# Optimization experiments

Hardware: AMD Instinct MI355X
Metric: run time of the kernel (lower is better)

## Reference

```python
import jax, jax.numpy as jnp
import numpy as np
from jax import lax

ORDER = 6
SAMPLES = 64
TOPK = 512
STRIDE = 2          # contour features are stride-2 w.r.t. input ('1' level)
NMS_THRESH = 0.2
REF_ITERS = 4
REF_MARGIN = 3.0
HC = WC = 256       # contour-feature grid
HF = WF = 512       # full-res (refinement) grid


def conv2d(x, w, b=None, pad=0):
    # x: [B,C,H,W], w: [O,I,kh,kw]
    y = lax.conv_general_dilated(x, w, (1, 1), [(pad, pad), (pad, pad)],
                                 dimension_numbers=("NCHW", "OIHW", "NCHW"))
    if b is not None:
        y = y + b[None, :, None, None]
    return y


def setup_inputs() -> dict:
    key = jax.random.key(0)
    ks = jax.random.split(key, 16)
    s = 0.05
    d = {
        "contour_features": jax.random.normal(ks[0], (4, 64, HC, WC), jnp.float32),
        "enc_score_features": jax.random.normal(ks[1], (4, 64, HC, WC), jnp.float32),
        "refinement_features": jax.random.normal(ks[2], (4, 32, HF, WF), jnp.float32),
        "enc_refinement_features": jax.random.normal(ks[3], (4, 32, HF, WF), jnp.float32),
        # learned params
        "w_score_reduce": jax.random.normal(ks[4], (64, 128, 1, 1)) * s,
        "w_score": jax.random.normal(ks[5], (2, 64, 7, 7)) * s,
        "b_score": jnp.zeros((2,), jnp.float32),
        "w_loc": jax.random.normal(ks[6], (2, 64, 7, 7)) * s,
        "b_loc": jnp.zeros((2,), jnp.float32),
        "w_fourier": jax.random.normal(ks[7], (ORDER * 4, 64, 7, 7)) * s,
        "b_fourier": jnp.zeros((ORDER * 4,), jnp.float32),
        "w_ref_reduce": jax.random.normal(ks[8], (32, 64, 1, 1)) * s,
        "w_ref": jax.random.normal(ks[9], (2, 32, 7, 7)) * s,
        "b_ref": jnp.zeros((2,), jnp.float32),
    }
    return d


def _pairwise_iou(boxes):
    # boxes: [K,4] as (x1,y1,x2,y2)
    x1, y1, x2, y2 = boxes[:, 0], boxes[:, 1], boxes[:, 2], boxes[:, 3]
    area = jnp.maximum(x2 - x1, 0.) * jnp.maximum(y2 - y1, 0.)
    ix1 = jnp.maximum(x1[:, None], x1[None, :])
    iy1 = jnp.maximum(y1[:, None], y1[None, :])
    ix2 = jnp.minimum(x2[:, None], x2[None, :])
    iy2 = jnp.minimum(y2[:, None], y2[None, :])
    inter = jnp.maximum(ix2 - ix1, 0.) * jnp.maximum(iy2 - iy1, 0.)
    union = area[:, None] + area[None, :] - inter
    return inter / jnp.maximum(union, 1e-8)


def _nms_keep(boxes, valid):
    # boxes sorted by descending score. Sequential greedy NMS.
    iou = _pairwise_iou(boxes)  # [K,K]
    idx = jnp.arange(TOPK)

    def body(i, keep):
        sup = (iou[i] > NMS_THRESH) & keep[i] & (idx > i)
        return keep & ~sup

    keep = lax.fori_loop(0, TOPK, body, valid)
    return keep


def _forward(contour_features, enc_score_features, refinement_features,
             enc_refinement_features, w_score_reduce, w_score, b_score,
             w_loc, b_loc, w_fourier, b_fourier, w_ref_reduce, w_ref, b_ref):
    B = contour_features.shape[0]
    # ---- dense heads (CPNCore.forward) ----
    sf = conv2d(jnp.concatenate([contour_features, enc_score_features], 1), w_score_reduce)
    score_logits = conv2d(sf, w_score, b_score, pad=3)            # [B,2,HC,WC]
    log_scores = jax.nn.log_softmax(score_logits, axis=1)
    locations = conv2d(contour_features, w_loc, b_loc, pad=3)     # [B,2,HC,WC]
    fourier = conv2d(contour_features, w_fourier, b_fourier, pad=3)  # [B,4*ORDER,HC,WC]

    rf = conv2d(jnp.concatenate([refinement_features, enc_refinement_features], 1), w_ref_reduce)
    refinement = jnp.tanh(conv2d(rf, w_ref, b_ref, pad=3)) * REF_MARGIN  # [B,2,HF,WF]

    # ---- proposal selection: top-K foreground scores ----
    fg = jnp.exp(log_scores[:, 1])                                # [B,HC,WC]
    fg_flat = fg.reshape(B, -1)
    top_scores, top_idx = lax.top_k(fg_flat, TOPK)                # [B,K] sorted desc
    valid = top_scores > 0.5                                      # score_thresh

    gy = (top_idx // WC).astype(jnp.float32)
    gx = (top_idx % WC).astype(jnp.float32)

    def gather_ch(t):  # t: [B,C,HC,WC] -> [B,K,C]
        C = t.shape[1]
        tf = t.reshape(B, C, -1)
        out = jnp.take_along_axis(tf, top_idx[:, None, :].repeat(C, axis=1), axis=2)
        return out.transpose(0, 2, 1)

    loc = gather_ch(locations)                                    # [B,K,2] (x,y offsets)
    fr = gather_ch(fourier).reshape(B, TOPK, ORDER, 4)            # a_x,b_x,a_y,b_y

    cx = (gx + loc[..., 0]) * STRIDE
    cy = (gy + loc[..., 1]) * STRIDE

    # ---- fourier -> contour sampling ----
    t = jnp.arange(SAMPLES, dtype=jnp.float32) / SAMPLES
    k = jnp.arange(1, ORDER + 1, dtype=jnp.float32)
    ang = 2.0 * jnp.pi * k[:, None] * t[None, :]                  # [ORDER,SAMPLES]
    cos, sin = jnp.cos(ang), jnp.sin(ang)
    px = jnp.einsum('bko,os->bks', fr[..., 0], cos) + jnp.einsum('bko,os->bks', fr[..., 1], sin)
    py = jnp.einsum('bko,os->bks', fr[..., 2], cos) + jnp.einsum('bko,os->bks', fr[..., 3], sin)
    contour = jnp.stack([px * STRIDE + cx[..., None], py * STRIDE + cy[..., None]], -1)  # [B,K,S,2]

    # ---- iterative local refinement (nearest-neighbor gather) ----
    ref_flat = refinement.reshape(B, 2, -1)
    for _ in range(REF_ITERS):
        xi = jnp.clip(jnp.round(contour[..., 0]), 0, WF - 1).astype(jnp.int32)
        yi = jnp.clip(jnp.round(contour[..., 1]), 0, HF - 1).astype(jnp.int32)
        flat = (yi * WF + xi).reshape(B, 1, -1)                   # [B,1,K*S]
        off = jnp.take_along_axis(ref_flat, flat.repeat(2, axis=1), axis=2)
        off = off.reshape(B, 2, TOPK, SAMPLES).transpose(0, 2, 3, 1)  # [B,K,S,2]
        contour = contour + off

    # ---- boxes + NMS ----
    boxes = jnp.concatenate([contour.min(axis=2), contour.max(axis=2)], -1)  # [B,K,4]
    keep = jax.vmap(_nms_keep)(boxes, valid)
    return contour, top_scores, keep, boxes


def reference(contour_features, enc_score_features, refinement_features,
              enc_refinement_features, w_score_reduce, w_score, b_score,
              w_loc, b_loc, w_fourier, b_fourier, w_ref_reduce, w_ref, b_ref):
    return _forward(contour_features, enc_score_features, refinement_features,
                    enc_refinement_features, w_score_reduce, w_score, b_score,
                    w_loc, b_loc, w_fourier, b_fourier, w_ref_reduce, w_ref, b_ref)
```

## Files before the change

### kernel.cpp

```cpp
#include <hip/hip_runtime.h>
#include <math.h>

#define WS_D     0ull
#define WS_REF   1048576ull
#define WS_SPART 9437184ull
#define WS_WSE   13631488ull
#define WS_WRE   13731840ull
#define WS_WG    13782016ull
#define WS_TIDX  14108160ull
#define WS_GATH  14116352ull
#define WS_TRIG  14329344ull
#define WS_CLIST 14332416ull
#define WS_CNT   14365184ull
#define WS_PAIRS 14365200ull
#define WS_WRE32 14430736ull
#define WS_WSE32 14455824ull
#define WS_END   14506000ull

__global__ __launch_bounds__(256) void cpn_prep_kernel(
    const float* __restrict__ w_score_reduce, const float* __restrict__ w_score,
    const float* __restrict__ w_loc, const float* __restrict__ w_fourier,
    const float* __restrict__ w_ref_reduce, const float* __restrict__ w_ref,
    double* __restrict__ wse, double* __restrict__ wre, float* __restrict__ wg,
    float* __restrict__ trig, float* __restrict__ wre32, float* __restrict__ wse32)
{
    int i = blockIdx.x * 256 + threadIdx.x;
    if (i < 12544) {
        int o = i / 6272;
        int rem = i % 6272;
        int c = rem / 49, r = rem % 49;
        double a = 0.0;
        for (int m = 0; m < 64; ++m)
            a += (double)w_score[(o*64 + m)*49 + r] * (double)w_score_reduce[m*128 + c];
        wse[i] = a;
    } else if (i < 12544 + 6272) {
        int t = i - 12544;
        int o = t / 3136;
        int rem = t % 3136;
        int c = rem / 49, r = rem % 49;
        double a = 0.0;
        for (int m = 0; m < 32; ++m)
            a += (double)w_ref[(o*32 + m)*49 + r] * (double)w_ref_reduce[m*64 + c];
        wre[t] = a;
    } else if (i < 12544 + 6272 + 81536) {
        int t = i - 18816;
        int tap = t / 26, o = t % 26;
        wg[t] = (o < 2) ? w_loc[o*3136 + tap] : w_fourier[(o - 2)*3136 + tap];
    } else if (i < 100352 + 768) {
        int t = i - 100352;
        int cs = t / 384;
        int k = (t % 384) / 64, s = t % 64;
        const float TWO_PI_F = (float)6.283185307179586;
        float a1 = TWO_PI_F * (float)(k + 1);
        float tf = (float)s * 0.015625f;
        float ang = a1 * tf;
        double av = (double)ang;
        trig[t] = (cs == 0) ? (float)cos(av) : (float)sin(av);
    } else if (i < 101120 + 6272) {
        int t = i - 101120;
        int c = t / 98, r98 = t % 98;
        int ky = r98 / 14, q = r98 % 14;
        int kx = q >> 1, o = q & 1;
        int rr = ky*7 + kx;
        double a = 0.0;
        for (int m = 0; m < 32; ++m)
            a += (double)w_ref[(o*32 + m)*49 + rr] * (double)w_ref_reduce[m*64 + c];
        wre32[t] = (float)a;
    } else if (i < 107392 + 12544) {
        int t = i - 107392;
        int c = t / 98, r98 = t % 98;
        int ky = r98 / 14, q = r98 % 14;
        int kx = q >> 1, o = q & 1;
        int rr = ky*7 + kx;
        double a = 0.0;
        for (int m = 0; m < 64; ++m)
            a += (double)w_score[(o*64 + m)*49 + rr] * (double)w_score_reduce[m*128 + c];
        wse32[t] = (float)a;
    }
}

__global__ __launch_bounds__(512) void cpn_score_dense_kernel(
    const float* __restrict__ cf, const float* __restrict__ esf,
    const float* __restrict__ wse32, float2* __restrict__ partial)
{
    __shared__ __align__(16) float4 patches[4][22][11];
    const int tid  = threadIdx.x;
    const int t2   = tid & 127;
    const int q    = tid >> 7;
    const int b    = blockIdx.z >> 1;
    const int srch = blockIdx.z & 1;
    const float* src = srch ? esf : cf;
    const float* sbase = src + ((size_t)(b*64 + q*16) << 16);
    const int row0 = blockIdx.y * 16;
    const int col0 = blockIdx.x * 32;
    const int tyg  = t2 >> 3;
    const int txg  = t2 & 7;
    const int cbase = srch*64 + q*16;

    int  st_r[2], st_f[2];
    long st_off[2];
    bool st_ok[2];
    #pragma unroll
    for (int k = 0; k < 2; ++k) {
        int i = k*128 + t2;
        int r = i / 10, f = i % 10;
        int gy = row0 - 3 + r, gx = col0 - 4 + 4*f;
        st_r[k] = r; st_f[k] = f;
        st_ok[k] = (i < 220) && ((unsigned)gy < 256u) && ((unsigned)gx < 253u);
        st_off[k] = (long)gy * 256 + gx;
    }

    float4 s4[2];
    #pragma unroll
    for (int k = 0; k < 2; ++k) {
        float4 v = {0.f,0.f,0.f,0.f};
        if (st_ok[k]) v = *reinterpret_cast<const float4*>(sbase + st_off[k]);
        s4[k] = v;
    }

    float acc0[4] = {0.f,0.f,0.f,0.f};
    float acc1[4] = {0.f,0.f,0.f,0.f};

    for (int c = 0; c < 16; ++c) {
        #pragma unroll
        for (int k = 0; k < 2; ++k) {
            int i = k*128 + t2;
            if (i < 220) patches[q][st_r[k]][st_f[k]] = s4[k];
        }
        __syncthreads();
        if (c + 1 < 16) {
            const float* sp = sbase + ((size_t)(c+1) << 16);
            #pragma unroll
            for (int k = 0; k < 2; ++k) {
                float4 v = {0.f,0.f,0.f,0.f};
                if (st_ok[k]) v = *reinterpret_cast<const float4*>(sp + st_off[k]);
                s4[k] = v;
            }
        }
        int cg = __builtin_amdgcn_readfirstlane(cbase + c);
        const float* wc = wse32 + cg*98;
        #pragma unroll
        for (int pr = 0; pr < 7; ++pr) {
            int row = tyg + pr;
            float4 A = patches[q][row][txg + 0];
            float4 B2 = patches[q][row][txg + 1];
            float4 C2 = patches[q][row][txg + 2];
            float rv[12] = {A.x,A.y,A.z,A.w,B2.x,B2.y,B2.z,B2.w,C2.x,C2.y,C2.z,C2.w};
            const float* wp = wc + pr*14;
            float wv[14];
            #pragma unroll
            for (int w = 0; w < 14; ++w) wv[w] = wp[w];
            #pragma unroll
            for (int kx = 0; kx < 7; ++kx) {
                float w0 = wv[2*kx], w1 = wv[2*kx+1];
                #pragma unroll
                for (int p = 0; p < 4; ++p) {
                    float v = rv[p + kx + 1];
                    acc0[p] = fmaf(w0, v, acc0[p]);
                    acc1[p] = fmaf(w1, v, acc1[p]);
                }
            }
        }
        __syncthreads();
    }

    float* cmb = reinterpret_cast<float*>(&patches[0][0][0]);
    if (q > 0) {
        int base = ((q-1)*128 + t2)*8;
        #pragma unroll
        for (int p = 0; p < 4; ++p) { cmb[base + p] = acc0[p]; cmb[base + 4 + p] = acc1[p]; }
    }
    __syncthreads();
    if (q == 0) {
        int y = row0 + tyg;
        #pragma unroll
        for (int p = 0; p < 4; ++p) {
            float s0 = acc0[p];
            float s1 = acc1[p];
            s0 += cmb[(0*128 + t2)*8 + p];      s1 += cmb[(0*128 + t2)*8 + 4 + p];
            s0 += cmb[(1*128 + t2)*8 + p];      s1 += cmb[(1*128 + t2)*8 + 4 + p];
            s0 += cmb[(2*128 + t2)*8 + p];      s1 += cmb[(2*128 + t2)*8 + 4 + p];
            int x = col0 + txg*4 + p;
            float2 v; v.x = s0; v.y = s1;
            partial[(size_t)(srch*4 + b)*65536 + y*256 + x] = v;
        }
    }
}

__global__ __launch_bounds__(256) void cpn_dcomb_kernel(
    const float2* __restrict__ partial, float* __restrict__ d)
{
    int i = blockIdx.x * 256 + threadIdx.x;
    int b = i >> 16, px = i & 65535;
    float2 p0 = partial[(size_t)b*65536 + px];
    float2 p1 = partial[(size_t)(4 + b)*65536 + px];
    float l0 = p0.x + p1.x;
    float l1 = p0.y + p1.y;
    d[i] = l1 - l0;
}

__global__ __launch_bounds__(512) void cpn_ref_conv_kernel(
    const float* __restrict__ rff, const float* __restrict__ erf,
    const float* __restrict__ wre32, const float* __restrict__ b_ref,
    float* __restrict__ refmap)
{
    __shared__ __align__(16) float4 patches[4][22][19];
    const int tid = threadIdx.x;
    const int t2  = tid & 127;
    const int q   = tid >> 7;
    const int b   = blockIdx.z;
    const int row0 = blockIdx.y * 16;
    const int col0 = blockIdx.x * 64;
    const int tyg = t2 & 15;
    const int txg = t2 >> 4;
    const float* sbase = ((q < 2) ? rff : erf) + ((size_t)(b*32 + (q & 1)*16) << 18);

    int  st_r[4], st_f[4];
    long st_off[4];
    bool st_ok[4];
    #pragma unroll
    for (int k = 0; k < 4; ++k) {
        int i = k*128 + t2;
        int r = i / 18, f = i % 18;
        int gy = row0 - 3 + r, gx = col0 - 4 + 4*f;
        st_r[k] = r; st_f[k] = f;
        st_ok[k] = (i < 396) && ((unsigned)gy < 512u) && ((unsigned)gx < 509u);
        st_off[k] = (long)gy * 512 + gx;
    }

    float4 s4[4];
    #pragma unroll
    for (int k = 0; k < 4; ++k) {
        float4 v = {0.f,0.f,0.f,0.f};
        if (st_ok[k]) v = *reinterpret_cast<const float4*>(sbase + st_off[k]);
        s4[k] = v;
    }

    float acc0[8] = {0,0,0,0,0,0,0,0};
    float acc1[8] = {0,0,0,0,0,0,0,0};

    for (int c = 0; c < 16; ++c) {
        #pragma unroll
        for (int k = 0; k < 4; ++k) {
            int i = k*128 + t2;
            if (i < 396) patches[q][st_r[k]][st_f[k]] = s4[k];
        }
        __syncthreads();
        if (c + 1 < 16) {
            const float* sp = sbase + ((size_t)(c+1) << 18);
            #pragma unroll
            for (int k = 0; k < 4; ++k) {
                float4 v = {0.f,0.f,0.f,0.f};
                if (st_ok[k]) v = *reinterpret_cast<const float4*>(sp + st_off[k]);
                s4[k] = v;
            }
        }
        int cg = __builtin_amdgcn_readfirstlane(q*16 + c);
        const float* wc = wre32 + cg*98;
        #pragma unroll
        for (int pr = 0; pr < 7; ++pr) {
            int row = tyg + pr;
            float4 A  = patches[q][row][2*txg + 0];
            float4 B2 = patches[q][row][2*txg + 1];
            float4 C2 = patches[q][row][2*txg + 2];
            float4 D2 = patches[q][row][2*txg + 3];
            float rv[16] = {A.x,A.y,A.z,A.w,B2.x,B2.y,B2.z,B2.w,
                            C2.x,C2.y,C2.z,C2.w,D2.x,D2.y,D2.z,D2.w};
            const float* wp = wc + pr*14;
            float wv[14];
            #pragma unroll
            for (int w = 0; w < 14; ++w) wv[w] = wp[w];
            #pragma unroll
            for (int kx = 0; kx < 7; ++kx) {
                float w0 = wv[2*kx], w1 = wv[2*kx+1];
                #pragma unroll
                for (int p = 0; p < 8; ++p) {
                    float v = rv[p + kx + 1];
                    acc0[p] = fmaf(w0, v, acc0[p]);
                    acc1[p] = fmaf(w1, v, acc1[p]);
                }
            }
        }
        __syncthreads();
    }

    float* cmb = reinterpret_cast<float*>(&patches[0][0][0]);
    if (q > 0) {
        int base = ((q-1)*128 + t2)*16;
        #pragma unroll
        for (int p = 0; p < 8; ++p) { cmb[base + p] = acc0[p]; cmb[base + 8 + p] = acc1[p]; }
    }
    __syncthreads();
    if (q == 0) {
        float br0 = b_ref[0], br1 = b_ref[1];
        int y = row0 + tyg;
        int x0 = col0 + txg*8;
        #pragma unroll
        for (int p = 0; p < 8; ++p) {
            float s0 = acc0[p];
            float s1 = acc1[p];
            s0 += cmb[(0*128 + t2)*16 + p];      s1 += cmb[(0*128 + t2)*16 + 8 + p];
            s0 += cmb[(1*128 + t2)*16 + p];      s1 += cmb[(1*128 + t2)*16 + 8 + p];
            s0 += cmb[(2*128 + t2)*16 + p];      s1 += cmb[(2*128 + t2)*16 + 8 + p];
            refmap[((size_t)(b*2 + 0)*512 + y)*512 + x0 + p] = tanhf(s0 + br0) * 3.0f;
            refmap[((size_t)(b*2 + 1)*512 + y)*512 + x0 + p] = tanhf(s1 + br1) * 3.0f;
        }
    }
}

__device__ __forceinline__ void cpn_find_bucket(
    unsigned int* hist, unsigned int* seg, int nb, int target, int tid,
    int* s_bsel, int* s_cnt)
{
    int nseg = nb / 32;
    for (int t = tid; t < nseg; t += 1024) {
        unsigned int s = 0;
        for (int q = 0; q < 32; ++q) s += hist[t*32 + q];
        seg[t] = s;
    }
    __syncthreads();
    if (tid == 0) {
        int cum = 0, sg = 0;
        for (int jj = nseg - 1; jj >= 0; --jj) {
            int c = (int)seg[jj];
            if (cum + c >= target) { sg = jj; break; }
            cum += c;
        }
        int bs = sg*32;
        for (int jj = sg*32 + 31; jj >= sg*32; --jj) {
            int c = (int)hist[jj];
            if (cum + c >= target) { bs = jj; break; }
            cum += c;
        }
        *s_bsel = bs; *s_cnt = cum;
    }
    __syncthreads();
}

__device__ __forceinline__ unsigned int cpn_fkey(float v) {
    unsigned int u = __float_as_uint(v);
    return (u & 0x80000000u) ? ~u : (u | 0x80000000u);
}

__global__ __launch_bounds__(1024) void cpn_select_kernel(
    const float* __restrict__ d, int* __restrict__ clist, int* __restrict__ cnt)
{
    const int b = blockIdx.x;
    const int tid = threadIdx.x;
    const float* f = d + (size_t)b * 65536;

    __shared__ unsigned int hist[2048];
    __shared__ unsigned int seg[64];
    __shared__ int s_b, s_c, s_n;

    const int bitsA[3]  = {11,11,10};
    const int shiftA[3] = {21,10,0};

    unsigned int prefix = 0;
    int target = 512;
    for (int pass = 0; pass < 3; ++pass) {
        int sh = shiftA[pass], nb = 1 << bitsA[pass];
        for (int i = tid; i < 2048; i += 1024) hist[i] = 0;
        __syncthreads();
        if (pass == 0) {
            for (int i = tid; i < 65536; i += 1024) {
                unsigned int k = cpn_fkey(f[i]);
                atomicAdd(&hist[k >> 21], 1u);
            }
        } else {
            int hs = sh + bitsA[pass];
            for (int i = tid; i < 65536; i += 1024) {
                unsigned int k = cpn_fkey(f[i]);
                if ((k >> hs) == prefix)
                    atomicAdd(&hist[(k >> sh) & (nb-1)], 1u);
            }
        }
        __syncthreads();
        cpn_find_bucket(hist, seg, nb, target, tid, &s_b, &s_c);
        prefix = (prefix << bitsA[pass]) | (unsigned)s_b;
        target -= s_c;
    }
    float T = (prefix & 0x80000000u) ? __uint_as_float(prefix & 0x7FFFFFFFu)
                                     : __uint_as_float(~prefix);
    float tval = T - 0.0625f;

    if (tid == 0) s_n = 0;
    __syncthreads();
    for (int i = tid; i < 65536; i += 1024) {
        if (f[i] >= tval) {
            int q = atomicAdd(&s_n, 1);
            if (q < 2048) clist[b*2048 + q] = i;
        }
    }
    __syncthreads();
    if (tid == 0) cnt[b] = (s_n > 2048) ? 2048 : s_n;
}

__global__ __launch_bounds__(256) void cpn_recompute_kernel(
    const float* __restrict__ cf, const float* __restrict__ esf,
    const double* __restrict__ wse, const float* __restrict__ b_score,
    const int* __restrict__ clist, const int* __restrict__ cnt,
    uint2* __restrict__ pairs)
{
    const int b = blockIdx.y, q = blockIdx.x, tid = threadIdx.x;
    const int n = cnt[b];
    if (q >= n) {
        if (tid == 0) { uint2 pd; pd.x = 0u; pd.y = 0x7FFFFFFFu; pairs[b*2048 + q] = pd; }
        return;
    }
    const int idx = clist[b*2048 + q];
    const int gy = idx >> 8, gx = idx & 255;

    double L0 = 0.0, L1 = 0.0;
    for (int t = tid; t < 6272; t += 256) {
        int c = t / 49, r = t % 49, ky = r / 7, kx = r % 7;
        int y = gy + ky - 3, x = gx + kx - 3;
        float v = 0.f;
        if ((unsigned)y < 256u && (unsigned)x < 256u) {
            const float* src = (c < 64) ? cf : esf;
            v = src[((size_t)(b*64 + (c & 63)) << 16) + y*256 + x];
        }
        double dv = (double)v;
        L0 = fma(dv, wse[c*49 + r], L0);
        L1 = fma(dv, wse[6272 + c*49 + r], L1);
    }
    #pragma unroll
    for (int off = 32; off; off >>= 1) {
        L0 += __shfl_down(L0, off, 64);
        L1 += __shfl_down(L1, off, 64);
    }
    __shared__ double red[4][2];
    int w = tid >> 6, lane = tid & 63;
    if (lane == 0) { red[w][0] = L0; red[w][1] = L1; }
    __syncthreads();
    if (tid == 0) {
        double S0 = red[0][0] + red[1][0] + red[2][0] + red[3][0];
        double S1 = red[0][1] + red[1][1] + red[2][1] + red[3][1];
        float l0f = (float)(S0 + (double)b_score[0]);
        float l1f = (float)(S1 + (double)b_score[1]);
        float m  = fmaxf(l0f, l1f);
        float e0 = (float)exp((double)(l0f - m));
        float e1 = (float)exp((double)(l1f - m));
        float s  = e0 + e1;
        float lg = (float)log((double)s);
        float ls1 = (l1f - m) - lg;
        float fgv = (float)exp((double)ls1);
        uint2 pr; pr.x = __float_as_uint(fgv); pr.y = (unsigned)idx;
        pairs[b*2048 + q] = pr;
    }
}

__global__ __launch_bounds__(1024) void cpn_sortk_kernel(
    const uint2* __restrict__ pairs, int* __restrict__ tidx,
    float* __restrict__ tscores)
{
    const int b = blockIdx.x;
    const int tid = threadIdx.x;
    __shared__ unsigned int key[2048];
    __shared__ int sidx[2048];

    for (int q = tid; q < 2048; q += 1024) {
        uint2 pr = pairs[b*2048 + q];
        key[q] = pr.x; sidx[q] = (int)pr.y;
    }
    __syncthreads();
    for (int kk = 2; kk <= 2048; kk <<= 1)
        for (int jj = kk >> 1; jj > 0; jj >>= 1) {
            for (int i = tid; i < 2048; i += 1024) {
                int ixj = i ^ jj;
                if (ixj > i) {
                    unsigned int ka = key[i], kc = key[ixj];
                    int ia = sidx[i], ic = sidx[ixj];
                    bool up = ((i & kk) == 0);
                    bool aBefore = (ka > kc) || (ka == kc && ia < ic);
                    if (up ? !aBefore : aBefore) {
                        key[i] = kc; key[ixj] = ka;
                        sidx[i] = ic; sidx[ixj] = ia;
                    }
                }
            }
            __syncthreads();
        }
    for (int q = tid; q < 512; q += 1024) {
        tscores[b*512 + q] = __uint_as_float(key[q]);
        tidx[b*512 + q] = sidx[q];
    }
}

__global__ __launch_bounds__(256) void cpn_gather_conv_kernel(
    const float* __restrict__ cf, const float* __restrict__ wg,
    const float* __restrict__ b_loc, const float* __restrict__ b_fourier,
    const int* __restrict__ tidx, float* __restrict__ gath)
{
    const int b = blockIdx.y, p = blockIdx.x, tid = threadIdx.x;
    const int idx = tidx[b*512 + p];
    const int gy = idx >> 8, gx = idx & 255;

    double part[26];
    #pragma unroll
    for (int o = 0; o < 26; ++o) part[o] = 0.0;

    for (int t = tid; t < 3136; t += 256) {
        int c = t / 49, rr = t % 49, ky = rr / 7, kx = rr % 7;
        int y = gy + ky - 3, x = gx + kx - 3;
        float v = 0.f;
        if ((unsigned)y < 256u && (unsigned)x < 256u)
            v = cf[((size_t)(b*64 + c)*256 + y)*256 + x];
        const float* wr = wg + t*26;
        double dv = (double)v;
        #pragma unroll
        for (int o = 0; o < 26; ++o) part[o] = fma(dv, (double)wr[o], part[o]);
    }
    #pragma unroll
    for (int o = 0; o < 26; ++o)
        for (int off = 32; off; off >>= 1) part[o] += __shfl_down(part[o], off, 64);

    __shared__ double red[4][26];
    int w = tid >> 6, lane = tid & 63;
    if (lane == 0) {
        #pragma unroll
        for (int o = 0; o < 26; ++o) red[w][o] = part[o];
    }
    __syncthreads();
    if (tid < 26) {
        double s = red[0][tid] + red[1][tid] + red[2][tid] + red[3][tid];
        s += (tid < 2) ? (double)b_loc[tid] : (double)b_fourier[tid - 2];
        gath[((size_t)b*512 + p)*26 + tid] = (float)s;
    }
}

__global__ __launch_bounds__(64) void cpn_contour_kernel(
    const float* __restrict__ gath, const int* __restrict__ tidx,
    const float* __restrict__ refmap, const float* __restrict__ trig,
    float* __restrict__ out_contour, float* __restrict__ out_boxes)
{
    const int bp = blockIdx.x;
    const int b = bp >> 9;
    const int s = threadIdx.x;
    const float* g = gath + (size_t)bp * 26;
    const int idx = tidx[bp];
    const int gy = idx >> 8, gx = idx & 255;

    float cx = ((float)gx + g[0]) * 2.0f;
    float cy = ((float)gy + g[1]) * 2.0f;

    float sxc = 0.f, sxs = 0.f, syc = 0.f, sys = 0.f;
    #pragma unroll
    for (int k = 0; k < 6; ++k) {
        float cs = trig[k*64 + s];
        float sn = trig[384 + k*64 + s];
        float t0 = g[2 + k*4 + 0] * cs; asm volatile("" : "+v"(t0)); sxc += t0;
        float t1 = g[2 + k*4 + 1] * sn; asm volatile("" : "+v"(t1)); sxs += t1;
        float t2 = g[2 + k*4 + 2] * cs; asm volatile("" : "+v"(t2)); syc += t2;
        float t3 = g[2 + k*4 + 3] * sn; asm volatile("" : "+v"(t3)); sys += t3;
    }
    float px = sxc + sxs;
    float py = syc + sys;
    float x = px * 2.0f; asm volatile("" : "+v"(x)); x += cx;
    float y = py * 2.0f; asm volatile("" : "+v"(y)); y += cy;

    const float* r0 = refmap + (size_t)b * 2 * 262144;
    const float* r1 = r0 + 262144;
    #pragma unroll
    for (int it = 0; it < 4; ++it) {
        float xr = rintf(x); xr = fminf(fmaxf(xr, 0.f), 511.f);
        float yr = rintf(y); yr = fminf(fmaxf(yr, 0.f), 511.f);
        int xi = (int)xr, yi = (int)yr;
        x += r0[yi*512 + xi];
        y += r1[yi*512 + xi];
    }

    out_contour[((size_t)bp*64 + s)*2 + 0] = x;
    out_contour[((size_t)bp*64 + s)*2 + 1] = y;

    float mnx = x, mxx = x, mny = y, mxy = y;
    #pragma unroll
    for (int off = 32; off; off >>= 1) {
        mnx = fminf(mnx, __shfl_xor(mnx, off, 64));
        mny = fminf(mny, __shfl_xor(mny, off, 64));
        mxx = fmaxf(mxx, __shfl_xor(mxx, off, 64));
        mxy = fmaxf(mxy, __shfl_xor(mxy, off, 64));
    }
    if (s == 0) {
        out_boxes[bp*4 + 0] = mnx;
        out_boxes[bp*4 + 1] = mny;
        out_boxes[bp*4 + 2] = mxx;
        out_boxes[bp*4 + 3] = mxy;
    }
}

__global__ __launch_bounds__(512) void cpn_nms_kernel(
    const float* __restrict__ boxes, const float* __restrict__ scores,
    float* __restrict__ keep_out)
{
    const int b = blockIdx.x;
    const int j = threadIdx.x;
    __shared__ float X1[512], Y1[512], X2[512], Y2[512], AR[512];
    __shared__ int keep[512];

    const float* bb = boxes + b*512*4;
    float x1 = bb[j*4+0], y1 = bb[j*4+1], x2 = bb[j*4+2], y2 = bb[j*4+3];
    float aj = fmaxf(x2 - x1, 0.f) * fmaxf(y2 - y1, 0.f);
    X1[j] = x1; Y1[j] = y1; X2[j] = x2; Y2[j] = y2; AR[j] = aj;
    keep[j] = (scores[b*512 + j] > 0.5f) ? 1 : 0;
    __syncthreads();

    for (int i = 0; i < 512; ++i) {
        if (keep[i] && j > i) {
            float ix1 = fmaxf(x1, X1[i]);
            float iy1 = fmaxf(y1, Y1[i]);
            float ix2 = fminf(x2, X2[i]);
            float iy2 = fminf(y2, Y2[i]);
            float inter = fmaxf(ix2 - ix1, 0.f) * fmaxf(iy2 - iy1, 0.f);
            float uni = (aj + AR[i]) - inter;
            float iou = inter / fmaxf(uni, 1e-8f);
            if (iou > 0.2f) keep[j] = 0;
        }
        __syncthreads();
    }
    keep_out[b*512 + j] = keep[j] ? 1.0f : 0.0f;
}

extern "C" void kernel_launch(void* const* d_in, const int* in_sizes, int n_in,
                              void* d_out, int out_size, void* d_ws, size_t ws_size,
                              hipStream_t stream)
{
    if (ws_size < WS_END) return;

    const float* cf   = (const float*)d_in[0];
    const float* esf  = (const float*)d_in[1];
    const float* rff  = (const float*)d_in[2];
    const float* erf  = (const float*)d_in[3];
    const float* w_sr = (const float*)d_in[4];
    const float* w_s  = (const float*)d_in[5];
    const float* b_s  = (const float*)d_in[6];
    const float* w_l  = (const float*)d_in[7];
    const float* b_l  = (const float*)d_in[8];
    const float* w_f  = (const float*)d_in[9];
    const float* b_f  = (const float*)d_in[10];
    const float* w_rr = (const float*)d_in[11];
    const float* w_r  = (const float*)d_in[12];
    const float* b_r  = (const float*)d_in[13];

    char* ws = (char*)d_ws;
    float*  dbuf = (float*)(ws + WS_D);
    float*  refm = (float*)(ws + WS_REF);
    float2* spart = (float2*)(ws + WS_SPART);
    double* wse  = (double*)(ws + WS_WSE);
    double* wre  = (double*)(ws + WS_WRE);
    float*  wg   = (float*)(ws + WS_WG);
    int*    tidx = (int*)(ws + WS_TIDX);
    float*  gath = (float*)(ws + WS_GATH);
    float*  trig = (float*)(ws + WS_TRIG);
    int*    clist = (int*)(ws + WS_CLIST);
    int*    cnt  = (int*)(ws + WS_CNT);
    uint2*  pairs = (uint2*)(ws + WS_PAIRS);
    float*  wre32 = (float*)(ws + WS_WRE32);
    float*  wse32 = (float*)(ws + WS_WSE32);

    float* out_contour = (float*)d_out;
    float* out_scores  = out_contour + 262144;
    float* out_keep    = out_scores + 2048;
    float* out_boxes   = out_keep + 2048;

    cpn_prep_kernel<<<dim3(469), dim3(256), 0, stream>>>(
        w_sr, w_s, w_l, w_f, w_rr, w_r, wse, wre, wg, trig, wre32, wse32);
    cpn_score_dense_kernel<<<dim3(8, 16, 8), dim3(512), 0, stream>>>(
        cf, esf, wse32, spart);
    cpn_ref_conv_kernel<<<dim3(8, 32, 4), dim3(512), 0, stream>>>(
        rff, erf, wre32, b_r, refm);
    cpn_dcomb_kernel<<<dim3(1024), dim3(256), 0, stream>>>(spart, dbuf);
    cpn_select_kernel<<<dim3(4), dim3(1024), 0, stream>>>(dbuf, clist, cnt);
    cpn_recompute_kernel<<<dim3(2048, 4), dim3(256), 0, stream>>>(
        cf, esf, wse, b_s, clist, cnt, pairs);
    cpn_sortk_kernel<<<dim3(4), dim3(1024), 0, stream>>>(pairs, tidx, out_scores);
    cpn_gather_conv_kernel<<<dim3(512, 4), dim3(256), 0, stream>>>(
        cf, wg, b_l, b_f, tidx, gath);
    cpn_contour_kernel<<<dim3(2048), dim3(64), 0, stream>>>(
        gath, tidx, refm, trig, out_contour, out_boxes);
    cpn_nms_kernel<<<dim3(4), dim3(512), 0, stream>>>(
        out_boxes, out_scores, out_keep);
}
```

Measured before the change: 695.9 us.

## Merge score and refinement convolutions into one launch with double-buffered LDS tiles

The dense score conv and the refinement conv now run as a single launch, with blockIdx.z choosing which conv a block computes. This lets the two independent workloads share the GPU instead of running back to back. The refinement path now uses 32x64 tiles, splits channels into two halves of 32 instead of four of 16, and both paths double-buffer their LDS patches so each iteration needs one barrier instead of two. The costs are a larger shared-memory footprint that may lower occupancy, longer per-block serial channel loops on the refinement side, and a mixed grid whose blocks have uneven work.

```diff
diff --git a/kernel.cpp b/kernel.cpp
--- a/kernel.cpp
+++ b/kernel.cpp
@@ -79,110 +79,233 @@
     }
 }
 
-__global__ __launch_bounds__(512) void cpn_score_dense_kernel(
+__global__ __launch_bounds__(512) void cpn_dense_kernel(
+    const float* __restrict__ rff, const float* __restrict__ erf,
+    const float* __restrict__ wre32, const float* __restrict__ b_ref,
+    float* __restrict__ refmap,
     const float* __restrict__ cf, const float* __restrict__ esf,
     const float* __restrict__ wse32, float2* __restrict__ partial)
 {
-    __shared__ __align__(16) float4 patches[4][22][11];
-    const int tid  = threadIdx.x;
-    const int t2   = tid & 127;
-    const int q    = tid >> 7;
-    const int b    = blockIdx.z >> 1;
-    const int srch = blockIdx.z & 1;
-    const float* src = srch ? esf : cf;
-    const float* sbase = src + ((size_t)(b*64 + q*16) << 16);
-    const int row0 = blockIdx.y * 16;
-    const int col0 = blockIdx.x * 32;
-    const int tyg  = t2 >> 3;
-    const int txg  = t2 & 7;
-    const int cbase = srch*64 + q*16;
-
-    int  st_r[2], st_f[2];
-    long st_off[2];
-    bool st_ok[2];
-    #pragma unroll
-    for (int k = 0; k < 2; ++k) {
-        int i = k*128 + t2;
-        int r = i / 10, f = i % 10;
-        int gy = row0 - 3 + r, gx = col0 - 4 + 4*f;
-        st_r[k] = r; st_f[k] = f;
-        st_ok[k] = (i < 220) && ((unsigned)gy < 256u) && ((unsigned)gx < 253u);
-        st_off[k] = (long)gy * 256 + gx;
-    }
-
-    float4 s4[2];
-    #pragma unroll
-    for (int k = 0; k < 2; ++k) {
-        float4 v = {0.f,0.f,0.f,0.f};
-        if (st_ok[k]) v = *reinterpret_cast<const float4*>(sbase + st_off[k]);
-        s4[k] = v;
-    }
-
-    float acc0[4] = {0.f,0.f,0.f,0.f};
-    float acc1[4] = {0.f,0.f,0.f,0.f};
-
-    for (int c = 0; c < 16; ++c) {
+    __shared__ __align__(16) float4 ldsbuf[2][2][38][19];
+    const int tid = threadIdx.x;
+    const int z = blockIdx.z;
+
+    if (z < 4) {
+        const int t2  = tid & 255;
+        const int h   = tid >> 8;
+        const int b   = z;
+        const int row0 = blockIdx.y * 32;
+        const int col0 = blockIdx.x * 64;
+        const int tyg = t2 & 31;
+        const int txg = t2 >> 5;
+        const float* sbase = (h ? erf : rff) + ((size_t)(b*32) << 18);
+
+        int  st_r[3], st_f[3];
+        long st_off[3];
+        bool st_ok[3];
+        #pragma unroll
+        for (int k = 0; k < 3; ++k) {
+            int i = k*256 + t2;
+            int r = i / 18, f = i % 18;
+            int gy = row0 - 3 + r, gx = col0 - 4 + 4*f;
+            st_r[k] = r; st_f[k] = f;
+            st_ok[k] = (i < 684) && ((unsigned)gy < 512u) && ((unsigned)gx < 509u);
+            st_off[k] = (long)gy * 512 + gx;
+        }
+
+        float4 s4[3];
+        #pragma unroll
+        for (int k = 0; k < 3; ++k) {
+            float4 v = {0.f,0.f,0.f,0.f};
+            if (st_ok[k]) v = *reinterpret_cast<const float4*>(sbase + st_off[k]);
+            s4[k] = v;
+        }
+        #pragma unroll
+        for (int k = 0; k < 3; ++k) {
+            int i = k*256 + t2;
+            if (i < 684) ldsbuf[h][0][st_r[k]][st_f[k]] = s4[k];
+        }
+
+        float acc0[8] = {0,0,0,0,0,0,0,0};
+        float acc1[8] = {0,0,0,0,0,0,0,0};
+
+        for (int c = 0; c < 32; ++c) {
+            __syncthreads();
+            if (c + 1 < 32) {
+                const float* sp = sbase + ((size_t)(c+1) << 18);
+                #pragma unroll
+                for (int k = 0; k < 3; ++k) {
+                    float4 v = {0.f,0.f,0.f,0.f};
+                    if (st_ok[k]) v = *reinterpret_cast<const float4*>(sp + st_off[k]);
+                    s4[k] = v;
+                }
+            }
+            int cg = __builtin_amdgcn_readfirstlane(h*32 + c);
+            const float* wc = wre32 + cg*98;
+            const float4 (*pb)[19] = ldsbuf[h][c & 1];
+            #pragma unroll
+            for (int pr = 0; pr < 7; ++pr) {
+                int row = tyg + pr;
+                float4 A  = pb[row][2*txg + 0];
+                float4 B2 = pb[row][2*txg + 1];
+                float4 C2 = pb[row][2*txg + 2];
+                float4 D2 = pb[row][2*txg + 3];
+                float rv[16] = {A.x,A.y,A.z,A.w,B2.x,B2.y,B2.z,B2.w,
+                                C2.x,C2.y,C2.z,C2.w,D2.x,D2.y,D2.z,D2.w};
+                const float* wp = wc + pr*14;
+                float wv[14];
+                #pragma unroll
+                for (int w = 0; w < 14; ++w) wv[w] = wp[w];
+                #pragma unroll
+                for (int kx = 0; kx < 7; ++kx) {
+                    float w0 = wv[2*kx], w1 = wv[2*kx+1];
+                    #pragma unroll
+                    for (int p = 0; p < 8; ++p) {
+                        float v = rv[p + kx + 1];
+                        acc0[p] = fmaf(w0, v, acc0[p]);
+                        acc1[p] = fmaf(w1, v, acc1[p]);
+                    }
+                }
+            }
+            if (c + 1 < 32) {
+                #pragma unroll
+                for (int k = 0; k < 3; ++k) {
+                    int i = k*256 + t2;
+                    if (i < 684) ldsbuf[h][(c+1) & 1][st_r[k]][st_f[k]] = s4[k];
+                }
+            }
+        }
+        __syncthreads();
+
+        float* cmb = reinterpret_cast<float*>(&ldsbuf[0][0][0][0]);
+        if (h == 1) {
+            #pragma unroll
+            for (int p = 0; p < 8; ++p) { cmb[t2*16 + p] = acc0[p]; cmb[t2*16 + 8 + p] = acc1[p]; }
+        }
+        __syncthreads();
+        if (h == 0) {
+            float br0 = b_ref[0], br1 = b_ref[1];
+            int y = row0 + tyg;
+            int x0 = col0 + txg*8;
+            #pragma unroll
+            for (int p = 0; p < 8; ++p) {
+                float s0 = acc0[p] + cmb[t2*16 + p];
+                float s1 = acc1[p] + cmb[t2*16 + 8 + p];
+                refmap[((size_t)(b*2 + 0)*512 + y)*512 + x0 + p] = tanhf(s0 + br0) * 3.0f;
+                refmap[((size_t)(b*2 + 1)*512 + y)*512 + x0 + p] = tanhf(s1 + br1) * 3.0f;
+            }
+        }
+    } else {
+        const int zz = z - 4;
+        const int t2   = tid & 127;
+        const int q    = tid >> 7;
+        const int b    = zz >> 1;
+        const int srch = zz & 1;
+        const float* src = srch ? esf : cf;
+        const float* sbase = src + ((size_t)(b*64 + q*16) << 16);
+        const int row0 = blockIdx.y * 16;
+        const int col0 = blockIdx.x * 32;
+        const int tyg  = t2 >> 3;
+        const int txg  = t2 & 7;
+        const int cbase = srch*64 + q*16;
+        float4 (*spatch)[2][22][11] =
+            reinterpret_cast<float4(*)[2][22][11]>(&ldsbuf[0][0][0][0]);
+
+        int  st_r[2], st_f[2];
+        long st_off[2];
+        bool st_ok[2];
         #pragma unroll
         for (int k = 0; k < 2; ++k) {
             int i = k*128 + t2;
-            if (i < 220) patches[q][st_r[k]][st_f[k]] = s4[k];
+            int r = i / 10, f = i % 10;
+            int gy = row0 - 3 + r, gx = col0 - 4 + 4*f;
+            st_r[k] = r; st_f[k] = f;
+            st_ok[k] = (i < 220) && ((unsigned)gy < 256u) && ((unsigned)gx < 253u);
+            st_off[k] = (long)gy * 256 + gx;
+        }
+
+        float4 s4[2];
+        #pragma unroll
+        for (int k = 0; k < 2; ++k) {
+            float4 v = {0.f,0.f,0.f,0.f};
+            if (st_ok[k]) v = *reinterpret_cast<const float4*>(sbase + st_off[k]);
+            s4[k] = v;
+        }
+        #pragma unroll
+        for (int k = 0; k < 2; ++k) {
+            int i = k*128 + t2;
+            if (i < 220) spatch[q][0][st_r[k]][st_f[k]] = s4[k];
+        }
+
+        float acc0[4] = {0.f,0.f,0.f,0.f};
+        float acc1[4] = {0.f,0.f,0.f,0.f};
+
+        for (int c = 0; c < 16; ++c) {
+            __syncthreads();
+            if (c + 1 < 16) {
+                const float* sp = sbase + ((size_t)(c+1) << 16);
+                #pragma unroll
+                for (int k = 0; k < 2; ++k) {
+                    float4 v = {0.f,0.f,0.f,0.f};
+                    if (st_ok[k]) v = *reinterpret_cast<const float4*>(sp + st_off[k]);
+                    s4[k] = v;
+                }
+            }
+            int cg = __builtin_amdgcn_readfirstlane(cbase + c);
+            const float* wc = wse32 + cg*98;
+            const float4 (*pb)[11] = spatch[q][c & 1];
+            #pragma unroll
+            for (int pr = 0; pr < 7; ++pr) {
+                int row = tyg + pr;
+                float4 A  = pb[row][txg + 0];
+                float4 B2 = pb[row][txg + 1];
+                float4 C2 = pb[row][txg + 2];
+                float rv[12] = {A.x,A.y,A.z,A.w,B2.x,B2.y,B2.z,B2.w,C2.x,C2.y,C2.z,C2.w};
+                const float* wp = wc + pr*14;
+                float wv[14];
+                #pragma unroll
+                for (int w = 0; w < 14; ++w) wv[w] = wp[w];
+                #pragma unroll
+                for (int kx = 0; kx < 7; ++kx) {
+                    float w0 = wv[2*kx], w1 = wv[2*kx+1];
+                    #pragma unroll
+                    for (int p = 0; p < 4; ++p) {
+                        float v = rv[p + kx + 1];
+                        acc0[p] = fmaf(w0, v, acc0[p]);
+                        acc1[p] = fmaf(w1, v, acc1[p]);
+                    }
+                }
+            }
+            if (c + 1 < 16) {
+                #pragma unroll
+                for (int k = 0; k < 2; ++k) {
+                    int i = k*128 + t2;
+                    if (i < 220) spatch[q][(c+1) & 1][st_r[k]][st_f[k]] = s4[k];
+                }
+            }
         }
         __syncthreads();
-        if (c + 1 < 16) {
-            const float* sp = sbase + ((size_t)(c+1) << 16);
+
+        float* cmb = reinterpret_cast<float*>(&ldsbuf[0][0][0][0]);
+        if (q > 0) {
+            int base = ((q-1)*128 + t2)*8;
             #pragma unroll
-            for (int k = 0; k < 2; ++k) {
-                float4 v = {0.f,0.f,0.f,0.f};
-                if (st_ok[k]) v = *reinterpret_cast<const float4*>(sp + st_off[k]);
-                s4[k] = v;
-            }
-        }
-        int cg = __builtin_amdgcn_readfirstlane(cbase + c);
-        const float* wc = wse32 + cg*98;
-        #pragma unroll
-        for (int pr = 0; pr < 7; ++pr) {
-            int row = tyg + pr;
-            float4 A = patches[q][row][txg + 0];
-            float4 B2 = patches[q][row][txg + 1];
-            float4 C2 = patches[q][row][txg + 2];
-            float rv[12] = {A.x,A.y,A.z,A.w,B2.x,B2.y,B2.z,B2.w,C2.x,C2.y,C2.z,C2.w};
-            const float* wp = wc + pr*14;
-            float wv[14];
+            for (int p = 0; p < 4; ++p) { cmb[base + p] = acc0[p]; cmb[base + 4 + p] = acc1[p]; }
+        }
+        __syncthreads();
+        if (q == 0) {
+            int y = row0 + tyg;
             #pragma unroll
-            for (int w = 0; w < 14; ++w) wv[w] = wp[w];
-            #pragma unroll
-            for (int kx = 0; kx < 7; ++kx) {
-                float w0 = wv[2*kx], w1 = wv[2*kx+1];
-                #pragma unroll
-                for (int p = 0; p < 4; ++p) {
-                    float v = rv[p + kx + 1];
-                    acc0[p] = fmaf(w0, v, acc0[p]);
-                    acc1[p] = fmaf(w1, v, acc1[p]);
-                }
-            }
-        }
-        __syncthreads();
-    }
-
-    float* cmb = reinterpret_cast<float*>(&patches[0][0][0]);
-    if (q > 0) {
-        int base = ((q-1)*128 + t2)*8;
-        #pragma unroll
-        for (int p = 0; p < 4; ++p) { cmb[base + p] = acc0[p]; cmb[base + 4 + p] = acc1[p]; }
-    }
-    __syncthreads();
-    if (q == 0) {
-        int y = row0 + tyg;
-        #pragma unroll
-        for (int p = 0; p < 4; ++p) {
-            float s0 = acc0[p];
-            float s1 = acc1[p];
-            s0 += cmb[(0*128 + t2)*8 + p];      s1 += cmb[(0*128 + t2)*8 + 4 + p];
-            s0 += cmb[(1*128 + t2)*8 + p];      s1 += cmb[(1*128 + t2)*8 + 4 + p];
-            s0 += cmb[(2*128 + t2)*8 + p];      s1 += cmb[(2*128 + t2)*8 + 4 + p];
-            int x = col0 + txg*4 + p;
-            float2 v; v.x = s0; v.y = s1;
-            partial[(size_t)(srch*4 + b)*65536 + y*256 + x] = v;
+            for (int p = 0; p < 4; ++p) {
+                float s0 = acc0[p];
+                float s1 = acc1[p];
+                s0 += cmb[(0*128 + t2)*8 + p];      s1 += cmb[(0*128 + t2)*8 + 4 + p];
+                s0 += cmb[(1*128 + t2)*8 + p];      s1 += cmb[(1*128 + t2)*8 + 4 + p];
+                s0 += cmb[(2*128 + t2)*8 + p];      s1 += cmb[(2*128 + t2)*8 + 4 + p];
+                int x = col0 + txg*4 + p;
+                float2 v; v.x = s0; v.y = s1;
+                partial[(size_t)(srch*4 + b)*65536 + y*256 + x] = v;
+            }
         }
     }
 }
@@ -197,115 +320,6 @@
     float l0 = p0.x + p1.x;
     float l1 = p0.y + p1.y;
     d[i] = l1 - l0;
-}
-
-__global__ __launch_bounds__(512) void cpn_ref_conv_kernel(
-    const float* __restrict__ rff, const float* __restrict__ erf,
-    const float* __restrict__ wre32, const float* __restrict__ b_ref,
-    float* __restrict__ refmap)
-{
-    __shared__ __align__(16) float4 patches[4][22][19];
-    const int tid = threadIdx.x;
-    const int t2  = tid & 127;
-    const int q   = tid >> 7;
-    const int b   = blockIdx.z;
-    const int row0 = blockIdx.y * 16;
-    const int col0 = blockIdx.x * 64;
-    const int tyg = t2 & 15;
-    const int txg = t2 >> 4;
-    const float* sbase = ((q < 2) ? rff : erf) + ((size_t)(b*32 + (q & 1)*16) << 18);
-
-    int  st_r[4], st_f[4];
-    long st_off[4];
-    bool st_ok[4];
-    #pragma unroll
-    for (int k = 0; k < 4; ++k) {
-        int i = k*128 + t2;
-        int r = i / 18, f = i % 18;
-        int gy = row0 - 3 + r, gx = col0 - 4 + 4*f;
-        st_r[k] = r; st_f[k] = f;
-        st_ok[k] = (i < 396) && ((unsigned)gy < 512u) && ((unsigned)gx < 509u);
-        st_off[k] = (long)gy * 512 + gx;
-    }
-
-    float4 s4[4];
-    #pragma unroll
-    for (int k = 0; k < 4; ++k) {
-        float4 v = {0.f,0.f,0.f,0.f};
-        if (st_ok[k]) v = *reinterpret_cast<const float4*>(sbase + st_off[k]);
-        s4[k] = v;
-    }
-
-    float acc0[8] = {0,0,0,0,0,0,0,0};
-    float acc1[8] = {0,0,0,0,0,0,0,0};
-
-    for (int c = 0; c < 16; ++c) {
-        #pragma unroll
-        for (int k = 0; k < 4; ++k) {
-            int i = k*128 + t2;
-            if (i < 396) patches[q][st_r[k]][st_f[k]] = s4[k];
-        }
-        __syncthreads();
-        if (c + 1 < 16) {
-            const float* sp = sbase + ((size_t)(c+1) << 18);
-            #pragma unroll
-            for (int k = 0; k < 4; ++k) {
-                float4 v = {0.f,0.f,0.f,0.f};
-                if (st_ok[k]) v = *reinterpret_cast<const float4*>(sp + st_off[k]);
-                s4[k] = v;
-            }
-        }
-        int cg = __builtin_amdgcn_readfirstlane(q*16 + c);
-        const float* wc = wre32 + cg*98;
-        #pragma unroll
-        for (int pr = 0; pr < 7; ++pr) {
-            int row = tyg + pr;
-            float4 A  = patches[q][row][2*txg + 0];
-            float4 B2 = patches[q][row][2*txg + 1];
-            float4 C2 = patches[q][row][2*txg + 2];
-            float4 D2 = patches[q][row][2*txg + 3];
-            float rv[16] = {A.x,A.y,A.z,A.w,B2.x,B2.y,B2.z,B2.w,
-                            C2.x,C2.y,C2.z,C2.w,D2.x,D2.y,D2.z,D2.w};
-            const float* wp = wc + pr*14;
-            float wv[14];
-            #pragma unroll
-            for (int w = 0; w < 14; ++w) wv[w] = wp[w];
-            #pragma unroll
-            for (int kx = 0; kx < 7; ++kx) {
-                float w0 = wv[2*kx], w1 = wv[2*kx+1];
-                #pragma unroll
-                for (int p = 0; p < 8; ++p) {
-                    float v = rv[p + kx + 1];
-                    acc0[p] = fmaf(w0, v, acc0[p]);
-                    acc1[p] = fmaf(w1, v, acc1[p]);
-                }
-            }
-        }
-        __syncthreads();
-    }
-
-    float* cmb = reinterpret_cast<float*>(&patches[0][0][0]);
-    if (q > 0) {
-        int base = ((q-1)*128 + t2)*16;
-        #pragma unroll
-        for (int p = 0; p < 8; ++p) { cmb[base + p] = acc0[p]; cmb[base + 8 + p] = acc1[p]; }
-    }
-    __syncthreads();
-    if (q == 0) {
-        float br0 = b_ref[0], br1 = b_ref[1];
-        int y = row0 + tyg;
-        int x0 = col0 + txg*8;
-        #pragma unroll
-        for (int p = 0; p < 8; ++p) {
-            float s0 = acc0[p];
-            float s1 = acc1[p];
-            s0 += cmb[(0*128 + t2)*16 + p];      s1 += cmb[(0*128 + t2)*16 + 8 + p];
-            s0 += cmb[(1*128 + t2)*16 + p];      s1 += cmb[(1*128 + t2)*16 + 8 + p];
-            s0 += cmb[(2*128 + t2)*16 + p];      s1 += cmb[(2*128 + t2)*16 + 8 + p];
-            refmap[((size_t)(b*2 + 0)*512 + y)*512 + x0 + p] = tanhf(s0 + br0) * 3.0f;
-            refmap[((size_t)(b*2 + 1)*512 + y)*512 + x0 + p] = tanhf(s1 + br1) * 3.0f;
-        }
-    }
 }
 
 __device__ __forceinline__ void cpn_find_bucket(
@@ -665,10 +679,8 @@
 
     cpn_prep_kernel<<<dim3(469), dim3(256), 0, stream>>>(
         w_sr, w_s, w_l, w_f, w_rr, w_r, wse, wre, wg, trig, wre32, wse32);
-    cpn_score_dense_kernel<<<dim3(8, 16, 8), dim3(512), 0, stream>>>(
-        cf, esf, wse32, spart);
-    cpn_ref_conv_kernel<<<dim3(8, 32, 4), dim3(512), 0, stream>>>(
-        rff, erf, wre32, b_r, refm);
+    cpn_dense_kernel<<<dim3(8, 16, 12), dim3(512), 0, stream>>>(
+        rff, erf, wre32, b_r, refm, cf, esf, wse32, spart);
     cpn_dcomb_kernel<<<dim3(1024), dim3(256), 0, stream>>>(spart, dbuf);
     cpn_select_kernel<<<dim3(4), dim3(1024), 0, stream>>>(dbuf, clist, cnt);
     cpn_recompute_kernel<<<dim3(2048, 4), dim3(256), 0, stream>>>(
```

Result: slower. 766.1 us (+10.1%).
